# Kernel tuning notes

Hardware: AMD Instinct MI355X
Metric: run time of the kernel (lower is better)

## Reference

```python
import jax, jax.numpy as jnp
import numpy as np

N_NODES = 100000
N_EDGES = 1600000
IN_DIM, HID_DIM, OUT_DIM = 128, 128, 64


def setup_inputs() -> dict:
    key = jax.random.key(0)
    ks = jax.random.split(key, 5)
    x = jax.random.normal(ks[0], (N_NODES, IN_DIM), dtype=jnp.float32)
    edge_index = jax.random.randint(ks[1], (2, N_EDGES), 0, N_NODES, dtype=jnp.int64)
    W1 = jax.random.normal(ks[2], (IN_DIM, HID_DIM), dtype=jnp.float32) * (1.0 / np.sqrt(IN_DIM))
    b1 = jnp.zeros((HID_DIM,), dtype=jnp.float32)
    W2 = jax.random.normal(ks[3], (HID_DIM, OUT_DIM), dtype=jnp.float32) * (1.0 / np.sqrt(HID_DIM))
    b2 = jnp.zeros((OUT_DIM,), dtype=jnp.float32)
    return {"x": x, "edge_index": edge_index, "W1": W1, "b1": b1, "W2": W2, "b2": b2}


def _gcn_conv(h, row, col, norm, b, n_nodes):
    # h: [N, F] already linearly transformed; message = norm_e * h[src]; scatter-add to dst
    msg = h[row] * norm[:, None]                      # [E+N, F]
    out = jax.ops.segment_sum(msg, col, num_segments=n_nodes)
    return out + b


def reference(x, edge_index, W1, b1, W2, b2):
    n = x.shape[0]
    loops = jnp.arange(n, dtype=edge_index.dtype)
    row = jnp.concatenate([edge_index[0], loops])     # sources (incl. self loops)
    col = jnp.concatenate([edge_index[1], loops])     # targets
    # symmetric normalization: deg over targets with unit edge weights
    deg = jax.ops.segment_sum(jnp.ones_like(col, dtype=x.dtype), col, num_segments=n)
    dinv = jnp.where(deg > 0, jax.lax.rsqrt(jnp.maximum(deg, 1.0)), 0.0)
    norm = dinv[row] * dinv[col]                      # [E+N]
    h = jax.nn.relu(_gcn_conv(x @ W1, row, col, norm, b1, n))
    out = _gcn_conv(h @ W2, row, col, norm, b2, n)
    return out.mean(axis=0)                           # [OUT_DIM]
```

## Files before the change

kernel.cpp:

```cpp
#include <hip/hip_runtime.h>

#define N_NODES 100000
#define N_EDGES 1600000
#define IN_DIM 128
#define HID_DIM 128
#define OUT_DIM 64
#define BKT_SHIFT 7
#define BKT_SIZE 128
#define NBKT ((N_NODES + BKT_SIZE - 1) / BKT_SIZE)
#define B1 128
#define HIST_N (NBKT * B1)
#define HIST_N2 (2 * HIST_N)

typedef float v2f __attribute__((ext_vector_type(2)));

__device__ __forceinline__ void load4(const void* ei, int is64, int half, int base,
                                      int* v) {
  if (is64) {
    const long long* e = (const long long*)ei + (size_t)half * N_EDGES + base;
    longlong2 a = *(const longlong2*)e;
    longlong2 b = *(const longlong2*)(e + 2);
    v[0] = (int)a.x; v[1] = (int)a.y; v[2] = (int)b.x; v[3] = (int)b.y;
  } else {
    const int* e = (const int*)ei + (size_t)half * N_EDGES + base;
    int4 a = *(const int4*)e;
    v[0] = a.x; v[1] = a.y; v[2] = a.z; v[3] = a.w;
  }
}

__global__ void detect_kernel(const unsigned int* ei, int* flag, float* S) {
  __shared__ int nz;
  if (threadIdx.x == 0) nz = 0;
  __syncthreads();
  unsigned int v = ei[1 + 2 * threadIdx.x];
  if (v != 0u) nz = 1;
  if (threadIdx.x < HID_DIM) S[threadIdx.x] = 0.f;
  __syncthreads();
  if (threadIdx.x == 0) *flag = (nz == 0) ? 1 : 0;
}

__global__ __launch_bounds__(256) void hist_kernel(const void* ei, const int* flag,
                                                   int* hist) {
  __shared__ int hd[NBKT], hs[NBKT];
  for (int k = threadIdx.x; k < NBKT; k += 256) { hd[k] = 0; hs[k] = 0; }
  __syncthreads();
  const int is64 = *flag;
  for (int g = blockIdx.x * 256 + threadIdx.x; g < N_EDGES / 4; g += B1 * 256) {
    int r[4], c[4];
    load4(ei, is64, 0, g * 4, r);
    load4(ei, is64, 1, g * 4, c);
#pragma unroll
    for (int k = 0; k < 4; k++) {
      atomicAdd(&hd[c[k] >> BKT_SHIFT], 1);
      atomicAdd(&hs[r[k] >> BKT_SHIFT], 1);
    }
  }
  __syncthreads();
  for (int k = threadIdx.x; k < NBKT; k += 256) {
    hist[k * B1 + blockIdx.x] = hd[k];
    hist[HIST_N + k * B1 + blockIdx.x] = hs[k];
  }
}

__global__ void scan1_kernel(const int* cnt, int* part, int* bsum, int n) {
  __shared__ int tmp[256];
  int i = blockIdx.x * 256 + threadIdx.x;
  int v = (i < n) ? cnt[i] : 0;
  tmp[threadIdx.x] = v;
  __syncthreads();
  for (int off = 1; off < 256; off <<= 1) {
    int t2 = (threadIdx.x >= off) ? tmp[threadIdx.x - off] : 0;
    __syncthreads();
    tmp[threadIdx.x] += t2;
    __syncthreads();
  }
  if (i < n) part[i] = tmp[threadIdx.x] - v;
  if (threadIdx.x == 255) bsum[blockIdx.x] = tmp[255];
}

__global__ void scan2_kernel(int* bsum, int nb) {
  __shared__ int tmp[1024];
  int v = (threadIdx.x < nb) ? bsum[threadIdx.x] : 0;
  tmp[threadIdx.x] = v;
  __syncthreads();
  for (int off = 1; off < 1024; off <<= 1) {
    int t2 = (threadIdx.x >= off) ? tmp[threadIdx.x - off] : 0;
    __syncthreads();
    tmp[threadIdx.x] += t2;
    __syncthreads();
  }
  if (threadIdx.x < nb) bsum[threadIdx.x] = tmp[threadIdx.x] - v;
}

__global__ void scan3_kernel(int* arr, const int* bsum, int n) {
  int i = blockIdx.x * 256 + threadIdx.x;
  if (i < n) arr[i] += bsum[blockIdx.x];
}

__global__ __launch_bounds__(256) void scatter_kernel(const void* ei, const int* flag,
                                                      const int* hist,
                                                      unsigned int* pairs) {
  __shared__ int cd[NBKT], cs[NBKT];
  for (int k = threadIdx.x; k < NBKT; k += 256) {
    cd[k] = hist[k * B1 + blockIdx.x];
    cs[k] = hist[HIST_N + k * B1 + blockIdx.x];
  }
  __syncthreads();
  const int is64 = *flag;
  for (int g = blockIdx.x * 256 + threadIdx.x; g < N_EDGES / 4; g += B1 * 256) {
    int r[4], c[4];
    load4(ei, is64, 0, g * 4, r);
    load4(ei, is64, 1, g * 4, c);
#pragma unroll
    for (int k = 0; k < 4; k++) {
      int pd = atomicAdd(&cd[c[k] >> BKT_SHIFT], 1);
      pairs[pd] = ((unsigned int)(c[k] & (BKT_SIZE - 1)) << 17) | (unsigned int)r[k];
      int ps = atomicAdd(&cs[r[k] >> BKT_SHIFT], 1);
      pairs[ps] = ((unsigned int)(r[k] & (BKT_SIZE - 1)) << 17) | (unsigned int)c[k];
    }
  }
}

__global__ __launch_bounds__(256) void csr_kernel(const int* hist,
                                                  const unsigned int* pairs,
                                                  int* rowptr, int* csr, float* dinv) {
  __shared__ int cnt[BKT_SIZE], sc[BKT_SIZE], cur[BKT_SIZE];
  const int k = blockIdx.x;
  const int base = hist[k * B1];
  const int end = (k == NBKT - 1) ? N_EDGES : hist[(k + 1) * B1];
  const int nseg = end - base;
  const int l = threadIdx.x;
  if (l < BKT_SIZE) cnt[l] = 0;
  __syncthreads();
  for (int i = l; i < nseg; i += 256) atomicAdd(&cnt[pairs[base + i] >> 17], 1);
  __syncthreads();
  if (l < BKT_SIZE) sc[l] = cnt[l];
  __syncthreads();
  for (int off = 1; off < BKT_SIZE; off <<= 1) {
    int v = (l < BKT_SIZE && l >= off) ? sc[l - off] : 0;
    __syncthreads();
    if (l < BKT_SIZE) sc[l] += v;
    __syncthreads();
  }
  if (l < BKT_SIZE) {
    int excl = sc[l] - cnt[l];
    cur[l] = base + excl;
    int v = k * BKT_SIZE + l;
    if (v < N_NODES) {
      rowptr[v] = base + excl;
      dinv[v] = rsqrtf((float)(cnt[l] + 1));
    }
  }
  if (k == NBKT - 1 && l == 0) rowptr[N_NODES] = N_EDGES;
  __syncthreads();
  for (int i = l; i < nseg; i += 256) {
    unsigned int pk = pairs[base + i];
    int pos = atomicAdd(&cur[pk >> 17], 1);
    csr[pos] = (int)(pk & 0x1FFFFu);
  }
}

__global__ __launch_bounds__(256) void outsum_kernel(const int* hist,
                                                     const unsigned int* pairs,
                                                     const float* __restrict__ dinv,
                                                     float* wacc) {
  __shared__ float fb[BKT_SIZE];
  const int k = blockIdx.x;
  const int base = hist[HIST_N + k * B1];
  const int end = (k == NBKT - 1) ? 2 * N_EDGES : hist[HIST_N + (k + 1) * B1];
  if (threadIdx.x < BKT_SIZE) fb[threadIdx.x] = 0.f;
  __syncthreads();
  for (int i = base + threadIdx.x; i < end; i += 256) {
    unsigned int pk = pairs[i];
    atomicAdd(&fb[pk >> 17], dinv[pk & 0x1FFFFu]);
  }
  __syncthreads();
  int v = k * BKT_SIZE + threadIdx.x;
  if (threadIdx.x < BKT_SIZE && v < N_NODES) wacc[v] = fb[threadIdx.x];
}

__global__ __launch_bounds__(256) void gemm_kernel(const float* __restrict__ x,
                                                   const float* __restrict__ W,
                                                   const float* __restrict__ dinv,
                                                   unsigned int* __restrict__ G) {
  __shared__ float lx[64 * IN_DIM];
  __shared__ float lw[32 * HID_DIM];
  const int t = threadIdx.x;
  const int row0 = blockIdx.x * 64;
  const int nrow = min(64, N_NODES - row0);

  {
    const float4* x4 = (const float4*)(x + (size_t)row0 * IN_DIM);
    float4* lx4 = (float4*)lx;
    const int tot = nrow * (IN_DIM / 4);
    for (int i = t; i < tot; i += 256) lx4[i] = x4[i];
  }

  const int c0 = (t & 31) * 4;
  const int rbase = (t >> 5) * 8;
  float4 acc[8];
#pragma unroll
  for (int i = 0; i < 8; i++) acc[i] = make_float4(0.f, 0.f, 0.f, 0.f);

  for (int kc = 0; kc < IN_DIM; kc += 32) {
    __syncthreads();
    {
      const float4* W4 = (const float4*)(W + (size_t)kc * HID_DIM);
      float4* lw4 = (float4*)lw;
      for (int i = t; i < 32 * HID_DIM / 4; i += 256) lw4[i] = W4[i];
    }
    __syncthreads();
#pragma unroll
    for (int kk = 0; kk < 32; kk += 4) {
      float4 xv[8];
#pragma unroll
      for (int i = 0; i < 8; i++)
        xv[i] = *(const float4*)&lx[(rbase + i) * IN_DIM + kc + kk];
#pragma unroll
      for (int j = 0; j < 4; j++) {
        float4 wv = *(const float4*)&lw[(kk + j) * HID_DIM + c0];
#pragma unroll
        for (int i = 0; i < 8; i++) {
          float xs = (j == 0) ? xv[i].x : (j == 1) ? xv[i].y : (j == 2) ? xv[i].z : xv[i].w;
          acc[i].x += xs * wv.x;
          acc[i].y += xs * wv.y;
          acc[i].z += xs * wv.z;
          acc[i].w += xs * wv.w;
        }
      }
    }
  }
#pragma unroll
  for (int i = 0; i < 8; i++) {
    int r = row0 + rbase + i;
    if (r < N_NODES) {
      float d = dinv[r];
      float4 v = acc[i];
      int pk = __builtin_amdgcn_cvt_pk_fp8_f32(v.x * d, v.y * d, 0, false);
      pk = __builtin_amdgcn_cvt_pk_fp8_f32(v.z * d, v.w * d, pk, true);
      G[(size_t)r * (HID_DIM / 4) + (c0 >> 2)] = (unsigned int)pk;
    }
  }
}

__global__ __launch_bounds__(256) void aggregate_kernel(
    const unsigned short* __restrict__ G, const int* __restrict__ rowptr,
    const int* __restrict__ csr, const float* __restrict__ dinv,
    const float* __restrict__ wacc, const float* __restrict__ b1,
    float* __restrict__ S) {
  const int lane = threadIdx.x & 63;
  const int wid = blockIdx.x * (blockDim.x >> 6) + (threadIdx.x >> 6);
  const int nwaves = gridDim.x * (blockDim.x >> 6);
  const float2 b = ((const float2*)b1)[lane];
  float2 sacc = make_float2(0.f, 0.f);

  for (int c = wid; c < N_NODES; c += nwaves) {
    const int start = rowptr[c];
    const int cnum = rowptr[c + 1] - start;
    v2f acc = __builtin_amdgcn_cvt_pk_f32_fp8((int)G[(size_t)c * 64 + lane], false);
    for (int j0 = 0; j0 < cnum; j0 += 64) {
      int src = 0;
      if (j0 + lane < cnum) src = csr[start + j0 + lane];
      const int m = min(64, cnum - j0);
      int i = 0;
      for (; i + 4 <= m; i += 4) {
        int s0 = __shfl(src, i);
        int s1 = __shfl(src, i + 1);
        int s2 = __shfl(src, i + 2);
        int s3 = __shfl(src, i + 3);
        int g0 = G[(size_t)s0 * 64 + lane];
        int g1 = G[(size_t)s1 * 64 + lane];
        int g2 = G[(size_t)s2 * 64 + lane];
        int g3 = G[(size_t)s3 * 64 + lane];
        v2f f0 = __builtin_amdgcn_cvt_pk_f32_fp8(g0, false);
        v2f f1 = __builtin_amdgcn_cvt_pk_f32_fp8(g1, false);
        v2f f2 = __builtin_amdgcn_cvt_pk_f32_fp8(g2, false);
        v2f f3 = __builtin_amdgcn_cvt_pk_f32_fp8(g3, false);
        acc += (f0 + f1) + (f2 + f3);
      }
      for (; i < m; i++) {
        int s = __shfl(src, i);
        acc += __builtin_amdgcn_cvt_pk_f32_fp8((int)G[(size_t)s * 64 + lane], false);
      }
    }
    float d = dinv[c];
    float hx = fmaxf(fmaf(d, acc.x, b.x), 0.f);
    float hy = fmaxf(fmaf(d, acc.y, b.y), 0.f);
    float wc = d * (wacc[c] + d);
    sacc.x += wc * hx;
    sacc.y += wc * hy;
  }

  __shared__ float ls[HID_DIM];
  if (threadIdx.x < HID_DIM) ls[threadIdx.x] = 0.f;
  __syncthreads();
  atomicAdd(&ls[2 * lane], sacc.x);
  atomicAdd(&ls[2 * lane + 1], sacc.y);
  __syncthreads();
  if (threadIdx.x < HID_DIM) atomicAdd(&S[threadIdx.x], ls[threadIdx.x]);
}

__global__ void finish_kernel(const float* __restrict__ S, const float* __restrict__ W2,
                              const float* __restrict__ b2, float* __restrict__ out) {
  int j = threadIdx.x;
  float acc = 0.f;
  for (int k = 0; k < HID_DIM; k++) acc += S[k] * W2[k * OUT_DIM + j];
  out[j] = acc * (1.0f / N_NODES) + b2[j];
}

extern "C" void kernel_launch(void* const* d_in, const int* in_sizes, int n_in,
                              void* d_out, int out_size, void* d_ws, size_t ws_size,
                              hipStream_t stream) {
  const float* x  = (const float*)d_in[0];
  const void*  ei = d_in[1];
  const float* W1 = (const float*)d_in[2];
  const float* b1 = (const float*)d_in[3];
  const float* W2 = (const float*)d_in[4];
  const float* b2 = (const float*)d_in[5];
  float* out = (float*)d_out;

  char* p = (char*)d_ws;
  size_t off = 0;
  auto alloc = [&](size_t bytes) -> void* {
    void* r = p + off;
    off = (off + bytes + 63) & ~(size_t)63;
    return r;
  };
  int*   flag   = (int*)alloc(64);
  int*   hist   = (int*)alloc((size_t)HIST_N2 * 4);
  int*   bsum   = (int*)alloc(1024 * 4);
  unsigned int* pairs = (unsigned int*)alloc((size_t)2 * N_EDGES * 4);
  int*   rowptr = (int*)alloc(((size_t)N_NODES + 1) * 4);
  int*   csr    = (int*)alloc((size_t)N_EDGES * 4);
  float* dinv   = (float*)alloc((size_t)N_NODES * 4);
  float* wacc   = (float*)alloc((size_t)N_NODES * 4);
  float* S      = (float*)alloc(HID_DIM * 4);
  unsigned int* G = (unsigned int*)alloc((size_t)N_NODES * HID_DIM);
  (void)ws_size; (void)n_in; (void)in_sizes; (void)out_size;

  const int NBH = HIST_N2 / 256;

  detect_kernel<<<1, 256, 0, stream>>>((const unsigned int*)ei, flag, S);
  hist_kernel<<<B1, 256, 0, stream>>>(ei, flag, hist);
  scan1_kernel<<<NBH, 256, 0, stream>>>(hist, hist, bsum, HIST_N2);
  scan2_kernel<<<1, 1024, 0, stream>>>(bsum, NBH);
  scan3_kernel<<<NBH, 256, 0, stream>>>(hist, bsum, HIST_N2);
  scatter_kernel<<<B1, 256, 0, stream>>>(ei, flag, hist, pairs);
  csr_kernel<<<NBKT, 256, 0, stream>>>(hist, pairs, rowptr, csr, dinv);
  outsum_kernel<<<NBKT, 256, 0, stream>>>(hist, pairs, dinv, wacc);
  gemm_kernel<<<(N_NODES + 63) / 64, 256, 0, stream>>>(x, W1, dinv, G);
  aggregate_kernel<<<2048, 256, 0, stream>>>((const unsigned short*)G, rowptr, csr,
                                             dinv, wacc, b1, S);
  finish_kernel<<<1, 64, 0, stream>>>(S, W2, b2, out);
}
```

Before: 313.0 us.

## Split wave into half-waves gathering two neighbors with 4-byte loads; enlarge buckets

The aggregation kernel now has each half of a wave gather a different neighbor row. Each lane loads 4 fp8 values (a 32-bit word) instead of 2, so one wave instruction covers two 128-byte rows. The two halves' partial sums are combined with shuffles at the end. Separately, the bucket size and histogram block count are raised from 128 to 256, which fills all threads in the CSR and outsum kernels and halves the number of buckets. The goals are fewer gather instructions per edge and better thread use in bucketing, at the cost of extra shuffles and some idle half-waves on odd-degree tails.

```diff
diff --git a/kernel.cpp b/kernel.cpp
--- a/kernel.cpp
+++ b/kernel.cpp
@@ -5,10 +5,10 @@
 #define IN_DIM 128
 #define HID_DIM 128
 #define OUT_DIM 64
-#define BKT_SHIFT 7
-#define BKT_SIZE 128
+#define BKT_SHIFT 8
+#define BKT_SIZE 256
 #define NBKT ((N_NODES + BKT_SIZE - 1) / BKT_SIZE)
-#define B1 128
+#define B1 256
 #define HIST_N (NBKT * B1)
 #define HIST_N2 (2 * HIST_N)
 
@@ -130,19 +130,19 @@
   const int end = (k == NBKT - 1) ? N_EDGES : hist[(k + 1) * B1];
   const int nseg = end - base;
   const int l = threadIdx.x;
-  if (l < BKT_SIZE) cnt[l] = 0;
+  cnt[l] = 0;
   __syncthreads();
   for (int i = l; i < nseg; i += 256) atomicAdd(&cnt[pairs[base + i] >> 17], 1);
   __syncthreads();
-  if (l < BKT_SIZE) sc[l] = cnt[l];
+  sc[l] = cnt[l];
   __syncthreads();
   for (int off = 1; off < BKT_SIZE; off <<= 1) {
-    int v = (l < BKT_SIZE && l >= off) ? sc[l - off] : 0;
-    __syncthreads();
-    if (l < BKT_SIZE) sc[l] += v;
-    __syncthreads();
-  }
-  if (l < BKT_SIZE) {
+    int v = (l >= off) ? sc[l - off] : 0;
+    __syncthreads();
+    sc[l] += v;
+    __syncthreads();
+  }
+  {
     int excl = sc[l] - cnt[l];
     cur[l] = base + excl;
     int v = k * BKT_SIZE + l;
@@ -168,7 +168,7 @@
   const int k = blockIdx.x;
   const int base = hist[HIST_N + k * B1];
   const int end = (k == NBKT - 1) ? 2 * N_EDGES : hist[HIST_N + (k + 1) * B1];
-  if (threadIdx.x < BKT_SIZE) fb[threadIdx.x] = 0.f;
+  fb[threadIdx.x] = 0.f;
   __syncthreads();
   for (int i = base + threadIdx.x; i < end; i += 256) {
     unsigned int pk = pairs[i];
@@ -176,7 +176,7 @@
   }
   __syncthreads();
   int v = k * BKT_SIZE + threadIdx.x;
-  if (threadIdx.x < BKT_SIZE && v < N_NODES) wacc[v] = fb[threadIdx.x];
+  if (v < N_NODES) wacc[v] = fb[threadIdx.x];
 }
 
 __global__ __launch_bounds__(256) void gemm_kernel(const float* __restrict__ x,
@@ -244,58 +244,88 @@
 }
 
 __global__ __launch_bounds__(256) void aggregate_kernel(
-    const unsigned short* __restrict__ G, const int* __restrict__ rowptr,
+    const unsigned int* __restrict__ G, const int* __restrict__ rowptr,
     const int* __restrict__ csr, const float* __restrict__ dinv,
     const float* __restrict__ wacc, const float* __restrict__ b1,
     float* __restrict__ S) {
   const int lane = threadIdx.x & 63;
+  const int sub = lane & 31;
+  const int half = lane >> 5;
   const int wid = blockIdx.x * (blockDim.x >> 6) + (threadIdx.x >> 6);
   const int nwaves = gridDim.x * (blockDim.x >> 6);
-  const float2 b = ((const float2*)b1)[lane];
-  float2 sacc = make_float2(0.f, 0.f);
+  const float4 b = ((const float4*)b1)[sub];
+  v2f sacc01 = {0.f, 0.f}, sacc23 = {0.f, 0.f};
 
   for (int c = wid; c < N_NODES; c += nwaves) {
     const int start = rowptr[c];
     const int cnum = rowptr[c + 1] - start;
-    v2f acc = __builtin_amdgcn_cvt_pk_f32_fp8((int)G[(size_t)c * 64 + lane], false);
+    v2f a01 = {0.f, 0.f}, a23 = {0.f, 0.f};
+    if (half == 0) {
+      unsigned int g = G[c * 32 + sub];
+      a01 = __builtin_amdgcn_cvt_pk_f32_fp8((int)g, false);
+      a23 = __builtin_amdgcn_cvt_pk_f32_fp8((int)g, true);
+    }
     for (int j0 = 0; j0 < cnum; j0 += 64) {
       int src = 0;
       if (j0 + lane < cnum) src = csr[start + j0 + lane];
       const int m = min(64, cnum - j0);
       int i = 0;
-      for (; i + 4 <= m; i += 4) {
-        int s0 = __shfl(src, i);
-        int s1 = __shfl(src, i + 1);
-        int s2 = __shfl(src, i + 2);
-        int s3 = __shfl(src, i + 3);
-        int g0 = G[(size_t)s0 * 64 + lane];
-        int g1 = G[(size_t)s1 * 64 + lane];
-        int g2 = G[(size_t)s2 * 64 + lane];
-        int g3 = G[(size_t)s3 * 64 + lane];
-        v2f f0 = __builtin_amdgcn_cvt_pk_f32_fp8(g0, false);
-        v2f f1 = __builtin_amdgcn_cvt_pk_f32_fp8(g1, false);
-        v2f f2 = __builtin_amdgcn_cvt_pk_f32_fp8(g2, false);
-        v2f f3 = __builtin_amdgcn_cvt_pk_f32_fp8(g3, false);
-        acc += (f0 + f1) + (f2 + f3);
+      for (; i + 8 <= m; i += 8) {
+        int s0 = __shfl(src, i + half);
+        int s1 = __shfl(src, i + 2 + half);
+        int s2 = __shfl(src, i + 4 + half);
+        int s3 = __shfl(src, i + 6 + half);
+        unsigned int g0 = G[s0 * 32 + sub];
+        unsigned int g1 = G[s1 * 32 + sub];
+        unsigned int g2 = G[s2 * 32 + sub];
+        unsigned int g3 = G[s3 * 32 + sub];
+        a01 += __builtin_amdgcn_cvt_pk_f32_fp8((int)g0, false) +
+               __builtin_amdgcn_cvt_pk_f32_fp8((int)g1, false);
+        a23 += __builtin_amdgcn_cvt_pk_f32_fp8((int)g0, true) +
+               __builtin_amdgcn_cvt_pk_f32_fp8((int)g1, true);
+        a01 += __builtin_amdgcn_cvt_pk_f32_fp8((int)g2, false) +
+               __builtin_amdgcn_cvt_pk_f32_fp8((int)g3, false);
+        a23 += __builtin_amdgcn_cvt_pk_f32_fp8((int)g2, true) +
+               __builtin_amdgcn_cvt_pk_f32_fp8((int)g3, true);
       }
-      for (; i < m; i++) {
+      for (; i + 2 <= m; i += 2) {
+        int s = __shfl(src, i + half);
+        unsigned int g = G[s * 32 + sub];
+        a01 += __builtin_amdgcn_cvt_pk_f32_fp8((int)g, false);
+        a23 += __builtin_amdgcn_cvt_pk_f32_fp8((int)g, true);
+      }
+      if (i < m) {
         int s = __shfl(src, i);
-        acc += __builtin_amdgcn_cvt_pk_f32_fp8((int)G[(size_t)s * 64 + lane], false);
+        if (half == 0) {
+          unsigned int g = G[s * 32 + sub];
+          a01 += __builtin_amdgcn_cvt_pk_f32_fp8((int)g, false);
+          a23 += __builtin_amdgcn_cvt_pk_f32_fp8((int)g, true);
+        }
       }
     }
-    float d = dinv[c];
-    float hx = fmaxf(fmaf(d, acc.x, b.x), 0.f);
-    float hy = fmaxf(fmaf(d, acc.y, b.y), 0.f);
-    float wc = d * (wacc[c] + d);
-    sacc.x += wc * hx;
-    sacc.y += wc * hy;
+    a01.x += __shfl(a01.x, sub + 32);
+    a01.y += __shfl(a01.y, sub + 32);
+    a23.x += __shfl(a23.x, sub + 32);
+    a23.y += __shfl(a23.y, sub + 32);
+    if (half == 0) {
+      float d = dinv[c];
+      float wc = d * (wacc[c] + d);
+      sacc01.x += wc * fmaxf(fmaf(d, a01.x, b.x), 0.f);
+      sacc01.y += wc * fmaxf(fmaf(d, a01.y, b.y), 0.f);
+      sacc23.x += wc * fmaxf(fmaf(d, a23.x, b.z), 0.f);
+      sacc23.y += wc * fmaxf(fmaf(d, a23.y, b.w), 0.f);
+    }
   }
 
   __shared__ float ls[HID_DIM];
   if (threadIdx.x < HID_DIM) ls[threadIdx.x] = 0.f;
   __syncthreads();
-  atomicAdd(&ls[2 * lane], sacc.x);
-  atomicAdd(&ls[2 * lane + 1], sacc.y);
+  if (half == 0) {
+    atomicAdd(&ls[4 * sub + 0], sacc01.x);
+    atomicAdd(&ls[4 * sub + 1], sacc01.y);
+    atomicAdd(&ls[4 * sub + 2], sacc23.x);
+    atomicAdd(&ls[4 * sub + 3], sacc23.y);
+  }
   __syncthreads();
   if (threadIdx.x < HID_DIM) atomicAdd(&S[threadIdx.x], ls[threadIdx.x]);
 }
@@ -349,7 +379,6 @@
   csr_kernel<<<NBKT, 256, 0, stream>>>(hist, pairs, rowptr, csr, dinv);
   outsum_kernel<<<NBKT, 256, 0, stream>>>(hist, pairs, dinv, wacc);
   gemm_kernel<<<(N_NODES + 63) / 64, 256, 0, stream>>>(x, W1, dinv, G);
-  aggregate_kernel<<<2048, 256, 0, stream>>>((const unsigned short*)G, rowptr, csr,
-                                             dinv, wacc, b1, S);
+  aggregate_kernel<<<2048, 256, 0, stream>>>(G, rowptr, csr, dinv, wacc, b1, S);
   finish_kernel<<<1, 64, 0, stream>>>(S, W2, b2, out);
 }
```

After: 299.1 us. 1.05x faster.
